# Optimization experiments

Hardware: AMD Instinct MI355X
Metric: run time of the kernel (lower is better)

## Reference

```python
import jax, jax.numpy as jnp
import numpy as np

NUM_HEADS = 16

def setup_inputs() -> dict:
    key = jax.random.key(0)
    ks = jax.random.split(key, 4)
    D = 1024
    x = jax.random.normal(ks[0], (2, 8192, D), dtype=jnp.float32)
    s = 1.0 / np.sqrt(D)
    Wqkv = jax.random.normal(ks[1], (D, 3 * D), dtype=jnp.float32) * s
    Wq = jax.random.normal(ks[2], (D, D), dtype=jnp.float32) * s
    Wproj = jax.random.normal(ks[3], (D, D), dtype=jnp.float32) * s
    return {
        "x": x,
        "Wqkv": Wqkv, "bqkv": jnp.zeros((3 * D,), jnp.float32),
        "Wq": Wq, "bq": jnp.zeros((D,), jnp.float32),
        "Wproj": Wproj, "bproj": jnp.zeros((D,), jnp.float32),
        "num_anchor_tokens": 1024,
    }

def reference(x, Wqkv, bqkv, Wq, bq, Wproj, bproj, num_anchor_tokens):
    B, S, D = x.shape
    H = NUM_HEADS
    hd = D // H
    A = num_anchor_tokens
    scale = 1.0 / jnp.sqrt(jnp.float32(hd))

    anchors = x[:, :A, :]          # (B, A, D)
    queries = x[:, A:, :]          # (B, Sq, D)
    Sq = S - A

    # Anchor QKV projection: (B, A, 3, H, hd)
    aqkv = (anchors @ Wqkv + bqkv).reshape(B, A, 3, H, hd)
    aqkv = jnp.transpose(aqkv, (2, 0, 3, 1, 4))   # (3, B, H, A, hd)
    aq, ak, av = aqkv[0], aqkv[1], aqkv[2]

    # Query-token Q projection: (B, H, Sq, hd)
    qq = (queries @ Wq + bq).reshape(B, Sq, H, hd)
    qq = jnp.transpose(qq, (0, 2, 1, 3))

    q = jnp.concatenate([aq, qq], axis=2)         # (B, H, S, hd)

    # All queries attend only to anchor keys/values
    scores = jnp.einsum('bhqd,bhkd->bhqk', q, ak) * scale   # (B, H, S, A)
    attn = jax.nn.softmax(scores, axis=-1)
    out = jnp.einsum('bhqk,bhkd->bhqd', attn, av)           # (B, H, S, hd)

    out = jnp.transpose(out, (0, 2, 1, 3)).reshape(B, S, D)
    return out @ Wproj + bproj
```

## Files before the change

kernel.cpp:

```cpp
#include <hip/hip_runtime.h>
#include <cstdint>

#define B_ 2
#define S_ 8192
#define D_ 1024
#define H_ 16
#define HD_ 64
#define A_ 1024
#define SQ_ 7168

#define QSCALE 0.18033688011112042f

typedef unsigned short ushort_t;
typedef unsigned int uint_t;
typedef __bf16 bf16x8 __attribute__((ext_vector_type(8)));
typedef __bf16 bf16x4 __attribute__((ext_vector_type(4)));
typedef float floatx4 __attribute__((ext_vector_type(4)));
typedef ushort_t ushort8 __attribute__((ext_vector_type(8)));
typedef ushort_t ushort4v __attribute__((ext_vector_type(4)));

__device__ __forceinline__ ushort_t f2bf_c(float f) {
  __bf16 h = (__bf16)f;
  return __builtin_bit_cast(ushort_t, h);
}

__device__ __forceinline__ void glds16(const ushort_t* g, ushort_t* l) {
  __builtin_amdgcn_global_load_lds(
      (const __attribute__((address_space(1))) void*)g,
      (__attribute__((address_space(3))) void*)l, 16, 0, 0);
}

__global__ __launch_bounds__(256) void cvt_x(const float* __restrict__ x,
                                             ushort_t* __restrict__ xb) {
  int i = (blockIdx.x * 256 + threadIdx.x) * 8;
  float4 a = *(const float4*)(x + i);
  float4 b = *(const float4*)(x + i + 4);
  ushort8 o;
  o[0] = f2bf_c(a.x); o[1] = f2bf_c(a.y); o[2] = f2bf_c(a.z); o[3] = f2bf_c(a.w);
  o[4] = f2bf_c(b.x); o[5] = f2bf_c(b.y); o[6] = f2bf_c(b.z); o[7] = f2bf_c(b.w);
  *(ushort8*)(xb + i) = o;
}

__global__ __launch_bounds__(256) void cvt_w_all(
    const float* __restrict__ Wqkv, const float* __restrict__ Wq,
    const float* __restrict__ Wproj, ushort_t* __restrict__ wqkvT,
    ushort_t* __restrict__ wqT, ushort_t* __restrict__ wprojT) {
  __shared__ float t[32][33];
  const int z = blockIdx.z;
  const float* W;
  ushort_t* WT;
  int stride, colofs;
  if (z < 3)      { W = Wqkv;  WT = wqkvT + (size_t)z * 1024 * 1024; stride = 3072; colofs = z * 1024; }
  else if (z == 3){ W = Wq;    WT = wqT;    stride = 1024; colofs = 0; }
  else            { W = Wproj; WT = wprojT; stride = 1024; colofs = 0; }
  int n0 = blockIdx.x * 32, k0 = blockIdx.y * 32;
  int tx = threadIdx.x, ty = threadIdx.y;
  #pragma unroll
  for (int i = ty; i < 32; i += 8)
    t[i][tx] = W[(uint64_t)(k0 + i) * stride + colofs + n0 + tx];
  __syncthreads();
  #pragma unroll
  for (int i = ty; i < 32; i += 8)
    WT[(uint64_t)(n0 + i) * 1024 + k0 + tx] = f2bf_c(t[tx][i]);
}

__global__ __launch_bounds__(256) void gemm_qkvq(
    const ushort_t* __restrict__ xb, const ushort_t* __restrict__ wqkvT,
    const ushort_t* __restrict__ wqT, const float* __restrict__ bqkv,
    const float* __restrict__ bq, ushort_t* __restrict__ Qb,
    ushort_t* __restrict__ Kb, ushort_t* __restrict__ Vb) {
  __shared__ __align__(16) ushort_t At[2 * 128 * 32];
  __shared__ __align__(16) ushort_t Bt[2 * 128 * 32];
  const int t = threadIdx.x;
  const int lane = t & 63;
  const int quad = lane >> 4, ln = lane & 15;
  const int wave = t >> 6;
  const int wm = wave & 1, wn = wave >> 1;

  const int lin = blockIdx.x;
  const int id = (lin & 7) * 160 + (lin >> 3);
  const bool is0 = id < 384;
  int bx, by;
  if (is0) { bx = id & 15; by = id >> 4; }
  else     { int i2 = id - 384; bx = i2 % 112; by = i2 / 112; }
  const int m0 = bx * 128, n0 = by * 128;
  const ushort_t* WT = is0 ? wqkvT : wqT;
  const float* bias = is0 ? bqkv : bq;
  const int which = is0 ? (n0 >> 10) : -1;

  const int r0 = t >> 2, seg = t & 3;
  auto maprow = [&](int gm) -> int {
    if (is0) return (gm >> 10) * S_ + (gm & 1023);
    int bb = (gm >= SQ_) ? 1 : 0;
    return bb * S_ + A_ + (gm - bb * SQ_);
  };
  const ushort_t* arow0 = xb + (uint64_t)maprow(m0 + r0) * 1024;
  const ushort_t* arow1 = xb + (uint64_t)maprow(m0 + 64 + r0) * 1024;
  const ushort_t* brow0 = WT + (uint64_t)(n0 + r0) * 1024;
  const ushort_t* brow1 = WT + (uint64_t)(n0 + 64 + r0) * 1024;
  ushort_t* At_p0_lo = (ushort_t*)((char*)At + wave * 1024);
  ushort_t* At_p0_hi = (ushort_t*)((char*)At + 4096 + wave * 1024);
  ushort_t* At_p1_lo = (ushort_t*)((char*)At + 8192 + wave * 1024);
  ushort_t* At_p1_hi = (ushort_t*)((char*)At + 12288 + wave * 1024);
  ushort_t* Bt_p0_lo = (ushort_t*)((char*)Bt + wave * 1024);
  ushort_t* Bt_p0_hi = (ushort_t*)((char*)Bt + 4096 + wave * 1024);
  ushort_t* Bt_p1_lo = (ushort_t*)((char*)Bt + 8192 + wave * 1024);
  ushort_t* Bt_p1_hi = (ushort_t*)((char*)Bt + 12288 + wave * 1024);

  floatx4 acc[4][4];
  #pragma unroll
  for (int i = 0; i < 4; ++i)
    #pragma unroll
    for (int j = 0; j < 4; ++j) acc[i][j] = (floatx4)0.0f;

  for (int k0 = 0; k0 < 1024; k0 += 64) {
    __syncthreads();
    glds16(arow0 + k0 + seg * 8, At_p0_lo);
    glds16(arow1 + k0 + seg * 8, At_p0_hi);
    glds16(arow0 + k0 + 32 + seg * 8, At_p1_lo);
    glds16(arow1 + k0 + 32 + seg * 8, At_p1_hi);
    glds16(brow0 + k0 + seg * 8, Bt_p0_lo);
    glds16(brow1 + k0 + seg * 8, Bt_p0_hi);
    glds16(brow0 + k0 + 32 + seg * 8, Bt_p1_lo);
    glds16(brow1 + k0 + 32 + seg * 8, Bt_p1_hi);
    __syncthreads();
    #pragma unroll
    for (int ks = 0; ks < 2; ++ks) {
      bf16x8 af[4], bfr[4];
      #pragma unroll
      for (int i = 0; i < 4; ++i)
        af[i] = *(const bf16x8*)&At[ks * 4096 + (wm * 64 + i * 16 + ln) * 32 + quad * 8];
      #pragma unroll
      for (int j = 0; j < 4; ++j)
        bfr[j] = *(const bf16x8*)&Bt[ks * 4096 + (wn * 64 + j * 16 + ln) * 32 + quad * 8];
      #pragma unroll
      for (int i = 0; i < 4; ++i)
        #pragma unroll
        for (int j = 0; j < 4; ++j)
          acc[i][j] = __builtin_amdgcn_mfma_f32_16x16x32_bf16(af[i], bfr[j], acc[i][j], 0, 0, 0);
    }
  }

  if (which == 2) {
    #pragma unroll
    for (int i = 0; i < 4; ++i) {
      #pragma unroll
      for (int j = 0; j < 4; ++j) {
        int gm0 = m0 + wm * 64 + i * 16 + quad * 4;
        int gn = n0 + wn * 64 + j * 16 + ln;
        int bb = gm0 >> 10, a0 = gm0 & 1023;
        int h = (gn >> 6) & 15, d = gn & 63;
        float bi = bias[gn];
        ushort4v vv;
        #pragma unroll
        for (int r = 0; r < 4; ++r) vv[r] = f2bf_c(acc[i][j][r] + bi);
        *(ushort4v*)&Vb[((uint64_t)(bb * H_ + h) * HD_ + d) * A_ + a0] = vv;
      }
    }
  } else {
    #pragma unroll
    for (int i = 0; i < 4; ++i) {
      #pragma unroll
      for (int j = 0; j < 4; ++j) {
        #pragma unroll
        for (int r = 0; r < 4; ++r) {
          int gm = m0 + wm * 64 + i * 16 + quad * 4 + r;
          int gn = n0 + wn * 64 + j * 16 + ln;
          float v = acc[i][j][r] + bias[gn];
          if (is0) {
            int b = gm >> 10, a = gm & 1023;
            int h = (gn >> 6) & 15, d = gn & 63;
            if (which == 0)
              Qb[((uint64_t)(b * H_ + h) * S_ + a) * HD_ + d] = f2bf_c(v * QSCALE);
            else
              Kb[((uint64_t)(b * H_ + h) * A_ + a) * HD_ + d] = f2bf_c(v);
          } else {
            int b = (gm >= SQ_) ? 1 : 0; int sq = gm - b * SQ_;
            int h = gn >> 6, d = gn & 63;
            Qb[((uint64_t)(b * H_ + h) * S_ + (A_ + sq)) * HD_ + d] = f2bf_c(v * QSCALE);
          }
        }
      }
    }
  }
}

__global__ __launch_bounds__(256) void gemm_proj(
    const ushort_t* __restrict__ Ob, const ushort_t* __restrict__ WT,
    const float* __restrict__ bias, float* __restrict__ outf) {
  __shared__ __align__(16) ushort_t At[2 * 128 * 32];
  __shared__ __align__(16) ushort_t Bt[2 * 128 * 32];
  const int t = threadIdx.x;
  const int lane = t & 63;
  const int quad = lane >> 4, ln = lane & 15;
  const int wave = t >> 6;
  const int wm = wave & 1, wn = wave >> 1;

  const int lin = blockIdx.x + (int)blockIdx.y * 128;
  const int swz = (lin & 7) * 128 + (lin >> 3);
  const int m0 = (swz & 127) * 128, n0 = (swz >> 7) * 128;

  const int r0 = t >> 2, seg = t & 3;
  const ushort_t* arow0 = Ob + (uint64_t)(m0 + r0) * 1024;
  const ushort_t* arow1 = Ob + (uint64_t)(m0 + 64 + r0) * 1024;
  const ushort_t* brow0 = WT + (uint64_t)(n0 + r0) * 1024;
  const ushort_t* brow1 = WT + (uint64_t)(n0 + 64 + r0) * 1024;
  ushort_t* At_p0_lo = (ushort_t*)((char*)At + wave * 1024);
  ushort_t* At_p0_hi = (ushort_t*)((char*)At + 4096 + wave * 1024);
  ushort_t* At_p1_lo = (ushort_t*)((char*)At + 8192 + wave * 1024);
  ushort_t* At_p1_hi = (ushort_t*)((char*)At + 12288 + wave * 1024);
  ushort_t* Bt_p0_lo = (ushort_t*)((char*)Bt + wave * 1024);
  ushort_t* Bt_p0_hi = (ushort_t*)((char*)Bt + 4096 + wave * 1024);
  ushort_t* Bt_p1_lo = (ushort_t*)((char*)Bt + 8192 + wave * 1024);
  ushort_t* Bt_p1_hi = (ushort_t*)((char*)Bt + 12288 + wave * 1024);

  floatx4 acc[4][4];
  #pragma unroll
  for (int i = 0; i < 4; ++i)
    #pragma unroll
    for (int j = 0; j < 4; ++j) acc[i][j] = (floatx4)0.0f;

  for (int k0 = 0; k0 < 1024; k0 += 64) {
    __syncthreads();
    glds16(arow0 + k0 + seg * 8, At_p0_lo);
    glds16(arow1 + k0 + seg * 8, At_p0_hi);
    glds16(arow0 + k0 + 32 + seg * 8, At_p1_lo);
    glds16(arow1 + k0 + 32 + seg * 8, At_p1_hi);
    glds16(brow0 + k0 + seg * 8, Bt_p0_lo);
    glds16(brow1 + k0 + seg * 8, Bt_p0_hi);
    glds16(brow0 + k0 + 32 + seg * 8, Bt_p1_lo);
    glds16(brow1 + k0 + 32 + seg * 8, Bt_p1_hi);
    __syncthreads();
    #pragma unroll
    for (int ks = 0; ks < 2; ++ks) {
      bf16x8 af[4], bfr[4];
      #pragma unroll
      for (int i = 0; i < 4; ++i)
        af[i] = *(const bf16x8*)&At[ks * 4096 + (wm * 64 + i * 16 + ln) * 32 + quad * 8];
      #pragma unroll
      for (int j = 0; j < 4; ++j)
        bfr[j] = *(const bf16x8*)&Bt[ks * 4096 + (wn * 64 + j * 16 + ln) * 32 + quad * 8];
      #pragma unroll
      for (int i = 0; i < 4; ++i)
        #pragma unroll
        for (int j = 0; j < 4; ++j)
          acc[i][j] = __builtin_amdgcn_mfma_f32_16x16x32_bf16(af[i], bfr[j], acc[i][j], 0, 0, 0);
    }
  }

  #pragma unroll
  for (int i = 0; i < 4; ++i) {
    #pragma unroll
    for (int j = 0; j < 4; ++j) {
      #pragma unroll
      for (int r = 0; r < 4; ++r) {
        int gm = m0 + wm * 64 + i * 16 + quad * 4 + r;
        int gn = n0 + wn * 64 + j * 16 + ln;
        outf[(uint64_t)gm * 1024 + gn] = acc[i][j][r] + bias[gn];
      }
    }
  }
}

__global__ __launch_bounds__(256) void attn_mfma(const ushort_t* __restrict__ Qb,
                                                 const ushort_t* __restrict__ Kb,
                                                 const ushort_t* __restrict__ Vb,
                                                 ushort_t* __restrict__ Ob) {
  __shared__ __align__(16) ushort_t Ks[64 * 72];
  __shared__ __align__(16) ushort_t Vt[80 * 72];
  __shared__ __align__(16) ushort_t Ps[128 * 72];
  const int t = threadIdx.x;
  const int lane = t & 63;
  const int quad = lane >> 4, ln = lane & 15;
  const int wave = t >> 6;
  const int bh = blockIdx.y;
  const int b = bh >> 4, h = bh & 15;
  const int m0 = blockIdx.x * 128;

  bf16x8 qf[2][2];
  {
    const ushort_t* qbase = Qb + ((uint64_t)bh * S_ + m0 + wave * 32 + ln) * HD_ + quad * 8;
    #pragma unroll
    for (int j = 0; j < 2; ++j)
      #pragma unroll
      for (int ks = 0; ks < 2; ++ks)
        qf[j][ks] = *(const bf16x8*)(qbase + (uint64_t)(j * 16) * HD_ + ks * 32);
  }
  if (t < 64) Vt[64 * 72 + t] = 0x3F80;

  floatx4 oacc[2][5];
  #pragma unroll
  for (int i = 0; i < 2; ++i)
    #pragma unroll
    for (int j = 0; j < 5; ++j) oacc[i][j] = (floatx4)0.0f;

  const ushort_t* kcbase = Kb + (uint64_t)bh * A_ * HD_;
  const ushort_t* vcbase = Vb + (uint64_t)bh * HD_ * A_;
  const int srow = t >> 2, sseg = t & 3;

  for (int kc = 0; kc < 16; ++kc) {
    const ushort_t* kg = kcbase + (uint64_t)(kc * 64 + srow) * 64 + sseg * 16;
    const ushort_t* vg = vcbase + (uint64_t)srow * A_ + kc * 64 + sseg * 16;
    ushort8 k0 = *(const ushort8*)kg;
    ushort8 k1 = *(const ushort8*)(kg + 8);
    ushort8 v0 = *(const ushort8*)vg;
    ushort8 v1 = *(const ushort8*)(vg + 8);
    __syncthreads();
    *(ushort8*)&Ks[srow * 72 + sseg * 16] = k0;
    *(ushort8*)&Ks[srow * 72 + sseg * 16 + 8] = k1;
    *(ushort8*)&Vt[srow * 72 + sseg * 16] = v0;
    *(ushort8*)&Vt[srow * 72 + sseg * 16 + 8] = v1;
    __syncthreads();

    floatx4 sacc[4][2];
    #pragma unroll
    for (int i = 0; i < 4; ++i)
      #pragma unroll
      for (int j = 0; j < 2; ++j) sacc[i][j] = (floatx4)0.0f;
    __builtin_amdgcn_s_setprio(1);
    #pragma unroll
    for (int ks = 0; ks < 2; ++ks) {
      bf16x8 kf[4];
      #pragma unroll
      for (int i = 0; i < 4; ++i)
        kf[i] = *(const bf16x8*)&Ks[(i * 16 + ln) * 72 + ks * 32 + quad * 8];
      #pragma unroll
      for (int i = 0; i < 4; ++i)
        #pragma unroll
        for (int j = 0; j < 2; ++j)
          sacc[i][j] = __builtin_amdgcn_mfma_f32_16x16x32_bf16(kf[i], qf[j][ks], sacc[i][j], 0, 0, 0);
    }
    __builtin_amdgcn_s_setprio(0);
    #pragma unroll
    for (int i = 0; i < 4; ++i)
      #pragma unroll
      for (int j = 0; j < 2; ++j) {
        float p0 = __builtin_amdgcn_exp2f(sacc[i][j][0]);
        float p1 = __builtin_amdgcn_exp2f(sacc[i][j][1]);
        float p2 = __builtin_amdgcn_exp2f(sacc[i][j][2]);
        float p3 = __builtin_amdgcn_exp2f(sacc[i][j][3]);
        bf16x4 pv;
        pv[0] = (__bf16)p0; pv[1] = (__bf16)p1;
        pv[2] = (__bf16)p2; pv[3] = (__bf16)p3;
        int q = wave * 32 + j * 16 + ln;
        int key = i * 16 + quad * 4;
        *(bf16x4*)&Ps[q * 72 + key] = pv;
      }

    __builtin_amdgcn_s_setprio(1);
    #pragma unroll
    for (int ks = 0; ks < 2; ++ks) {
      bf16x8 af[2];
      #pragma unroll
      for (int i2 = 0; i2 < 2; ++i2)
        af[i2] = *(const bf16x8*)&Ps[(wave * 32 + i2 * 16 + ln) * 72 + ks * 32 + quad * 8];
      bf16x8 bv[5];
      #pragma unroll
      for (int j = 0; j < 5; ++j)
        bv[j] = *(const bf16x8*)&Vt[(j * 16 + ln) * 72 + ks * 32 + quad * 8];
      #pragma unroll
      for (int i2 = 0; i2 < 2; ++i2)
        #pragma unroll
        for (int j = 0; j < 5; ++j)
          oacc[i2][j] = __builtin_amdgcn_mfma_f32_16x16x32_bf16(af[i2], bv[j], oacc[i2][j], 0, 0, 0);
    }
    __builtin_amdgcn_s_setprio(0);
  }

  #pragma unroll
  for (int i2 = 0; i2 < 2; ++i2) {
    #pragma unroll
    for (int r = 0; r < 4; ++r) {
      float lsum = __shfl(oacc[i2][4][r], lane & 48);
      float inv = 1.0f / lsum;
      int qrow = m0 + wave * 32 + i2 * 16 + quad * 4 + r;
      ushort_t* op = Ob + ((uint64_t)b * S_ + qrow) * D_ + h * HD_;
      #pragma unroll
      for (int j = 0; j < 4; ++j)
        op[j * 16 + ln] = f2bf_c(oacc[i2][j][r] * inv);
    }
  }
}

extern "C" void kernel_launch(void* const* d_in, const int* in_sizes, int n_in,
                              void* d_out, int out_size, void* d_ws, size_t ws_size,
                              hipStream_t stream) {
  (void)in_sizes; (void)n_in; (void)out_size; (void)ws_size;
  const float* x     = (const float*)d_in[0];
  const float* Wqkv  = (const float*)d_in[1];
  const float* bqkv  = (const float*)d_in[2];
  const float* Wq    = (const float*)d_in[3];
  const float* bq    = (const float*)d_in[4];
  const float* Wproj = (const float*)d_in[5];
  const float* bproj = (const float*)d_in[6];
  float* out = (float*)d_out;

  char* ws = (char*)d_ws;
  ushort_t* xb     = (ushort_t*)ws; ws += (size_t)B_ * S_ * D_ * 2;
  ushort_t* wqkvT  = (ushort_t*)ws; ws += (size_t)3 * D_ * D_ * 2;
  ushort_t* wqT    = (ushort_t*)ws; ws += (size_t)D_ * D_ * 2;
  ushort_t* wprojT = (ushort_t*)ws; ws += (size_t)D_ * D_ * 2;
  ushort_t* Qb     = (ushort_t*)ws; ws += (size_t)B_ * H_ * S_ * HD_ * 2;
  ushort_t* Kb     = (ushort_t*)ws; ws += (size_t)B_ * H_ * A_ * HD_ * 2;
  ushort_t* Vb     = (ushort_t*)ws; ws += (size_t)B_ * H_ * A_ * HD_ * 2;
  ushort_t* Ob     = (ushort_t*)ws;

  cvt_x<<<dim3((B_ * S_ * D_) / (256 * 8)), dim3(256), 0, stream>>>(x, xb);
  cvt_w_all<<<dim3(32, 32, 5), dim3(32, 8), 0, stream>>>(
      Wqkv, Wq, Wproj, wqkvT, wqT, wprojT);

  gemm_qkvq<<<dim3(1280), dim3(256), 0, stream>>>(
      xb, wqkvT, wqT, bqkv, bq, Qb, Kb, Vb);
  attn_mfma<<<dim3(S_ / 128, B_ * H_), dim3(256), 0, stream>>>(Qb, Kb, Vb, Ob);
  gemm_proj<<<dim3(128, 8), dim3(256), 0, stream>>>(Ob, wprojT, bproj, out);
}
```

Before: 377.7 us.

## Double-buffer LDS tiles in QKV and projection GEMMs to overlap loads

Both bf16 MFMA GEMM kernels now use the two LDS halves as ping-pong buffers with a K-step of 32. Each iteration issues the global-to-LDS copy for the next slice before the MFMAs on the current one, with a single barrier per step. This aims to hide global load latency behind matrix math instead of stalling at a barrier before every compute phase. The number of barriers stays about the same, but each iteration has less compute to cover the load. Correctness depends on the async LDS loads being complete when the barrier is reached.

```diff
diff --git a/kernel.cpp b/kernel.cpp
--- a/kernel.cpp
+++ b/kernel.cpp
@@ -98,14 +98,15 @@
   const ushort_t* arow1 = xb + (uint64_t)maprow(m0 + 64 + r0) * 1024;
   const ushort_t* brow0 = WT + (uint64_t)(n0 + r0) * 1024;
   const ushort_t* brow1 = WT + (uint64_t)(n0 + 64 + r0) * 1024;
-  ushort_t* At_p0_lo = (ushort_t*)((char*)At + wave * 1024);
-  ushort_t* At_p0_hi = (ushort_t*)((char*)At + 4096 + wave * 1024);
-  ushort_t* At_p1_lo = (ushort_t*)((char*)At + 8192 + wave * 1024);
-  ushort_t* At_p1_hi = (ushort_t*)((char*)At + 12288 + wave * 1024);
-  ushort_t* Bt_p0_lo = (ushort_t*)((char*)Bt + wave * 1024);
-  ushort_t* Bt_p0_hi = (ushort_t*)((char*)Bt + 4096 + wave * 1024);
-  ushort_t* Bt_p1_lo = (ushort_t*)((char*)Bt + 8192 + wave * 1024);
-  ushort_t* Bt_p1_hi = (ushort_t*)((char*)Bt + 12288 + wave * 1024);
+
+  auto stage = [&](int b, int k0) {
+    char* a_lo = (char*)At + b * 8192 + wave * 1024;
+    char* b_lo = (char*)Bt + b * 8192 + wave * 1024;
+    glds16(arow0 + k0 + seg * 8, (ushort_t*)a_lo);
+    glds16(arow1 + k0 + seg * 8, (ushort_t*)(a_lo + 4096));
+    glds16(brow0 + k0 + seg * 8, (ushort_t*)b_lo);
+    glds16(brow1 + k0 + seg * 8, (ushort_t*)(b_lo + 4096));
+  };
 
   floatx4 acc[4][4];
   #pragma unroll
@@ -113,32 +114,24 @@
     #pragma unroll
     for (int j = 0; j < 4; ++j) acc[i][j] = (floatx4)0.0f;
 
-  for (int k0 = 0; k0 < 1024; k0 += 64) {
+  stage(0, 0);
+  __syncthreads();
+  for (int it = 0; it < 32; ++it) {
+    const int cur = it & 1;
+    if (it + 1 < 32) stage(cur ^ 1, (it + 1) * 32);
+    bf16x8 af[4], bfr[4];
+    #pragma unroll
+    for (int i = 0; i < 4; ++i)
+      af[i] = *(const bf16x8*)&At[cur * 4096 + (wm * 64 + i * 16 + ln) * 32 + quad * 8];
+    #pragma unroll
+    for (int j = 0; j < 4; ++j)
+      bfr[j] = *(const bf16x8*)&Bt[cur * 4096 + (wn * 64 + j * 16 + ln) * 32 + quad * 8];
+    #pragma unroll
+    for (int i = 0; i < 4; ++i)
+      #pragma unroll
+      for (int j = 0; j < 4; ++j)
+        acc[i][j] = __builtin_amdgcn_mfma_f32_16x16x32_bf16(af[i], bfr[j], acc[i][j], 0, 0, 0);
     __syncthreads();
-    glds16(arow0 + k0 + seg * 8, At_p0_lo);
-    glds16(arow1 + k0 + seg * 8, At_p0_hi);
-    glds16(arow0 + k0 + 32 + seg * 8, At_p1_lo);
-    glds16(arow1 + k0 + 32 + seg * 8, At_p1_hi);
-    glds16(brow0 + k0 + seg * 8, Bt_p0_lo);
-    glds16(brow1 + k0 + seg * 8, Bt_p0_hi);
-    glds16(brow0 + k0 + 32 + seg * 8, Bt_p1_lo);
-    glds16(brow1 + k0 + 32 + seg * 8, Bt_p1_hi);
-    __syncthreads();
-    #pragma unroll
-    for (int ks = 0; ks < 2; ++ks) {
-      bf16x8 af[4], bfr[4];
-      #pragma unroll
-      for (int i = 0; i < 4; ++i)
-        af[i] = *(const bf16x8*)&At[ks * 4096 + (wm * 64 + i * 16 + ln) * 32 + quad * 8];
-      #pragma unroll
-      for (int j = 0; j < 4; ++j)
-        bfr[j] = *(const bf16x8*)&Bt[ks * 4096 + (wn * 64 + j * 16 + ln) * 32 + quad * 8];
-      #pragma unroll
-      for (int i = 0; i < 4; ++i)
-        #pragma unroll
-        for (int j = 0; j < 4; ++j)
-          acc[i][j] = __builtin_amdgcn_mfma_f32_16x16x32_bf16(af[i], bfr[j], acc[i][j], 0, 0, 0);
-    }
   }
 
   if (which == 2) {
@@ -205,14 +198,15 @@
   const ushort_t* arow1 = Ob + (uint64_t)(m0 + 64 + r0) * 1024;
   const ushort_t* brow0 = WT + (uint64_t)(n0 + r0) * 1024;
   const ushort_t* brow1 = WT + (uint64_t)(n0 + 64 + r0) * 1024;
-  ushort_t* At_p0_lo = (ushort_t*)((char*)At + wave * 1024);
-  ushort_t* At_p0_hi = (ushort_t*)((char*)At + 4096 + wave * 1024);
-  ushort_t* At_p1_lo = (ushort_t*)((char*)At + 8192 + wave * 1024);
-  ushort_t* At_p1_hi = (ushort_t*)((char*)At + 12288 + wave * 1024);
-  ushort_t* Bt_p0_lo = (ushort_t*)((char*)Bt + wave * 1024);
-  ushort_t* Bt_p0_hi = (ushort_t*)((char*)Bt + 4096 + wave * 1024);
-  ushort_t* Bt_p1_lo = (ushort_t*)((char*)Bt + 8192 + wave * 1024);
-  ushort_t* Bt_p1_hi = (ushort_t*)((char*)Bt + 12288 + wave * 1024);
+
+  auto stage = [&](int b, int k0) {
+    char* a_lo = (char*)At + b * 8192 + wave * 1024;
+    char* b_lo = (char*)Bt + b * 8192 + wave * 1024;
+    glds16(arow0 + k0 + seg * 8, (ushort_t*)a_lo);
+    glds16(arow1 + k0 + seg * 8, (ushort_t*)(a_lo + 4096));
+    glds16(brow0 + k0 + seg * 8, (ushort_t*)b_lo);
+    glds16(brow1 + k0 + seg * 8, (ushort_t*)(b_lo + 4096));
+  };
 
   floatx4 acc[4][4];
   #pragma unroll
@@ -220,32 +214,24 @@
     #pragma unroll
     for (int j = 0; j < 4; ++j) acc[i][j] = (floatx4)0.0f;
 
-  for (int k0 = 0; k0 < 1024; k0 += 64) {
+  stage(0, 0);
+  __syncthreads();
+  for (int it = 0; it < 32; ++it) {
+    const int cur = it & 1;
+    if (it + 1 < 32) stage(cur ^ 1, (it + 1) * 32);
+    bf16x8 af[4], bfr[4];
+    #pragma unroll
+    for (int i = 0; i < 4; ++i)
+      af[i] = *(const bf16x8*)&At[cur * 4096 + (wm * 64 + i * 16 + ln) * 32 + quad * 8];
+    #pragma unroll
+    for (int j = 0; j < 4; ++j)
+      bfr[j] = *(const bf16x8*)&Bt[cur * 4096 + (wn * 64 + j * 16 + ln) * 32 + quad * 8];
+    #pragma unroll
+    for (int i = 0; i < 4; ++i)
+      #pragma unroll
+      for (int j = 0; j < 4; ++j)
+        acc[i][j] = __builtin_amdgcn_mfma_f32_16x16x32_bf16(af[i], bfr[j], acc[i][j], 0, 0, 0);
     __syncthreads();
-    glds16(arow0 + k0 + seg * 8, At_p0_lo);
-    glds16(arow1 + k0 + seg * 8, At_p0_hi);
-    glds16(arow0 + k0 + 32 + seg * 8, At_p1_lo);
-    glds16(arow1 + k0 + 32 + seg * 8, At_p1_hi);
-    glds16(brow0 + k0 + seg * 8, Bt_p0_lo);
-    glds16(brow1 + k0 + seg * 8, Bt_p0_hi);
-    glds16(brow0 + k0 + 32 + seg * 8, Bt_p1_lo);
-    glds16(brow1 + k0 + 32 + seg * 8, Bt_p1_hi);
-    __syncthreads();
-    #pragma unroll
-    for (int ks = 0; ks < 2; ++ks) {
-      bf16x8 af[4], bfr[4];
-      #pragma unroll
-      for (int i = 0; i < 4; ++i)
-        af[i] = *(const bf16x8*)&At[ks * 4096 + (wm * 64 + i * 16 + ln) * 32 + quad * 8];
-      #pragma unroll
-      for (int j = 0; j < 4; ++j)
-        bfr[j] = *(const bf16x8*)&Bt[ks * 4096 + (wn * 64 + j * 16 + ln) * 32 + quad * 8];
-      #pragma unroll
-      for (int i = 0; i < 4; ++i)
-        #pragma unroll
-        for (int j = 0; j < 4; ++j)
-          acc[i][j] = __builtin_amdgcn_mfma_f32_16x16x32_bf16(af[i], bfr[j], acc[i][j], 0, 0, 0);
-    }
   }
 
   #pragma unroll
```

New measurement: 377.6 us. Within noise of the previous version (-0.0%).
